# Optimization experiments

Hardware: AMD Instinct MI355X
Metric: run time of the kernel (lower is better)

The kernel has to match this reference:

```python
import jax, jax.numpy as jnp
import numpy as np


def _safe_inv(d):
    # 1/d with inf -> 0, as in PyG HypergraphConv
    return jnp.where(d > 0, 1.0 / jnp.maximum(d, 1e-30), 0.0)


def _hconv(x, W, b, node_idx, hedge_idx, num_hyperedges):
    """PyG HypergraphConv (use_attention=False, hyperedge_weight=1):
    out = D^-1 H B^-1 H^T (x W) + b
    """
    N = x.shape[0]
    xw = x @ W  # [N, F]
    ones = jnp.ones(node_idx.shape[0], dtype=x.dtype)
    D = _safe_inv(jax.ops.segment_sum(ones, node_idx, num_segments=N))
    B = _safe_inv(jax.ops.segment_sum(ones, hedge_idx, num_segments=num_hyperedges))
    # node -> hyperedge: mean of incident node features (norm B at target edge)
    e_feat = jax.ops.segment_sum(B[hedge_idx, None] * xw[node_idx], hedge_idx,
                                 num_segments=num_hyperedges)  # [M, F]
    # hyperedge -> node: degree-normalized sum (norm D at target node)
    out = jax.ops.segment_sum(D[node_idx, None] * e_feat[hedge_idx], node_idx,
                              num_segments=N)  # [N, F]
    return out + b


def _prelu(x, a):
    return jnp.where(x >= 0, x, a * x)


def setup_inputs() -> dict:
    key = jax.random.key(0)
    k = jax.random.split(key, 8)
    N, F, NNZ, M = 50000, 128, 800000, 5000
    x = jax.random.normal(k[0], (N, F), dtype=jnp.float32)
    node_idx = jax.random.randint(k[1], (NNZ,), 0, N)
    hedge_idx = jax.random.randint(k[2], (NNZ,), 0, M)
    scale = 1.0 / np.sqrt(F)
    W1 = jax.random.normal(k[3], (F, F), dtype=jnp.float32) * scale
    b1 = jnp.zeros((F,), dtype=jnp.float32)
    W2 = jax.random.normal(k[4], (F, F), dtype=jnp.float32) * scale
    b2 = jnp.zeros((F,), dtype=jnp.float32)
    prelu_a = jnp.asarray(0.25, dtype=jnp.float32)  # nn.PReLU default init
    return {"x": x, "W1": W1, "b1": b1, "W2": W2, "b2": b2,
            "prelu_a": prelu_a, "node_idx": node_idx, "hedge_idx": hedge_idx,
            "num_hyperedges": M}


def reference(x, W1, b1, W2, b2, prelu_a, node_idx, hedge_idx, num_hyperedges):
    out1 = _prelu(_hconv(x, W1, b1, node_idx, hedge_idx, num_hyperedges), prelu_a)
    out1 = _hconv(out1, W2, b2, node_idx, hedge_idx, num_hyperedges) + x
    return _prelu(out1, prelu_a)
```

## Files before the change

kernel.cpp:

```cpp
#include <hip/hip_runtime.h>


typedef __attribute__((ext_vector_type(8))) short bf16x8;
typedef __attribute__((ext_vector_type(4))) float f32x4;

#define CHUNK 4096

__device__ __forceinline__ float bf2f(ushort u) {
  union { uint i; float f; } v; v.i = ((uint)u) << 16; return v.f;
}
__device__ __forceinline__ ushort f2bf(float f) {
  union { uint i; float f; } v; v.f = f;
  uint b = v.i + 0x7FFFu + ((v.i >> 16) & 1u);
  return (ushort)(b >> 16);
}


__global__ __launch_bounds__(256) void init_cursors(int* __restrict__ cursH, int sbh,
                                                    int capH, int* __restrict__ cursN,
                                                    int sbn, int capN) {
  int t = threadIdx.x;
  if (t < sbh) cursH[t] = t * capH;
  if (t < sbn) cursN[t] = t * capN;
}

__global__ __launch_bounds__(256) void binA(const int* __restrict__ ni,
                                            const int* __restrict__ hi, int nnz,
                                            int* __restrict__ cursH,
                                            int* __restrict__ cursN,
                                            uint* __restrict__ tmpH,
                                            uint* __restrict__ tmpN,
                                            int sbh, int sbn) {
  __shared__ int hH[128], hN[128];
  int t = threadIdx.x, b = blockIdx.x;
  for (int i = t; i < sbh; i += 256) hH[i] = 0;
  for (int i = t; i < sbn; i += 256) hN[i] = 0;
  __syncthreads();
  int base = b * CHUNK;
  int lim = min(nnz, base + CHUNK);
  for (int i = base + t; i < lim; i += 256) {
    atomicAdd(&hH[hi[i] >> 6], 1);
    atomicAdd(&hN[ni[i] >> 9], 1);
  }
  __syncthreads();
  for (int i = t; i < sbh; i += 256) {
    int c = hH[i];
    hH[i] = c ? atomicAdd(&cursH[i], c) : 0;
  }
  for (int i = t; i < sbn; i += 256) {
    int c = hN[i];
    hN[i] = c ? atomicAdd(&cursN[i], c) : 0;
  }
  __syncthreads();
  for (int i = base + t; i < lim; i += 256) {
    uint n = (uint)ni[i], h = (uint)hi[i];
    int pH = atomicAdd(&hH[h >> 6], 1);
    tmpH[pH] = (h << 17) | n;
    int pN = atomicAdd(&hN[n >> 9], 1);
    tmpN[pN] = (n << 13) | h;
  }
}

__global__ __launch_bounds__(1024) void phaseB(
    const uint* __restrict__ tmpH, const int* __restrict__ cursH, int sbh, int capH,
    const uint* __restrict__ tmpN, const int* __restrict__ cursN, int sbn, int capN,
    int M, int N,
    uint* __restrict__ csrMn, int* __restrict__ offM, int* __restrict__ cntM,
    float* __restrict__ Bm,
    ushort* __restrict__ csrNh, int* __restrict__ offN, int* __restrict__ cntN,
    float* __restrict__ Dn) {
  __shared__ int hist[512], cur[512], wtot[8], wexcl8[8];
  int t = threadIdx.x, b = blockIdx.x, l = t & 63, w = t >> 6;
  if (b < sbh) {
    int base = b * capH;
    int end = cursH[b];
    if (t < 64) hist[t] = 0;
    __syncthreads();
    for (int i = base + t; i < end; i += 1024)
      atomicAdd(&hist[(tmpH[i] >> 17) & 63], 1);
    __syncthreads();
    if (t < 64) {
      int v = hist[t], x = v;
#pragma unroll
      for (int s = 1; s < 64; s <<= 1) {
        int u = __shfl_up(x, s, 64);
        if (t >= s) x += u;
      }
      int excl = x - v;
      int h = b * 64 + t;
      if (h < M) {
        offM[h] = base + excl;
        cntM[h] = v;
        Bm[h] = v > 0 ? 1.0f / (float)v : 0.0f;
      }
      cur[t] = base + excl;
    }
    __syncthreads();
    for (int i = base + t; i < end; i += 1024) {
      uint rec = tmpH[i];
      int pos = atomicAdd(&cur[(rec >> 17) & 63], 1);
      csrMn[pos] = rec & 0x1FFFFu;
    }
  } else {
    b -= sbh;
    int base = b * capN;
    int end = cursN[b];
    if (t < 512) hist[t] = 0;
    __syncthreads();
    for (int i = base + t; i < end; i += 1024)
      atomicAdd(&hist[(tmpN[i] >> 13) & 511], 1);
    __syncthreads();
    int v = 0, x = 0;
    if (t < 512) {
      v = hist[t]; x = v;
#pragma unroll
      for (int s = 1; s < 64; s <<= 1) {
        int u = __shfl_up(x, s, 64);
        if (l >= s) x += u;
      }
      if (l == 63) wtot[w] = x;
    }
    __syncthreads();
    if (t == 0) {
      int run = 0;
      for (int i = 0; i < 8; i++) { wexcl8[i] = run; run += wtot[i]; }
    }
    __syncthreads();
    if (t < 512) {
      int excl = wexcl8[w] + x - v;
      int n = b * 512 + t;
      if (n < N) {
        offN[n] = base + excl;
        cntN[n] = v;
        Dn[n] = v > 0 ? 1.0f / (float)v : 0.0f;
      }
      cur[t] = base + excl;
    }
    __syncthreads();
    for (int i = base + t; i < end; i += 1024) {
      uint rec = tmpN[i];
      int pos = atomicAdd(&cur[(rec >> 13) & 511], 1);
      csrNh[pos] = (ushort)(rec & 0x1FFFu);
    }
  }
}


__global__ __launch_bounds__(256) void convert_k(const float* __restrict__ x,
                                                 ushort* __restrict__ xb, int total) {
  int idx = (blockIdx.x * 256 + threadIdx.x) * 8;
  if (idx >= total) return;
  float4 f0 = *(const float4*)&x[idx];
  float4 f1 = *(const float4*)&x[idx + 4];
  bf16x8 o;
  o[0] = (short)f2bf(f0.x); o[1] = (short)f2bf(f0.y);
  o[2] = (short)f2bf(f0.z); o[3] = (short)f2bf(f0.w);
  o[4] = (short)f2bf(f1.x); o[5] = (short)f2bf(f1.y);
  o[6] = (short)f2bf(f1.z); o[7] = (short)f2bf(f1.w);
  *(bf16x8*)&xb[idx] = o;
}

__global__ __launch_bounds__(256) void edge_gather(const ushort* __restrict__ XIN,
                                                   const uint* __restrict__ src,
                                                   const int* __restrict__ off,
                                                   const int* __restrict__ cnt,
                                                   const float* __restrict__ Bm,
                                                   ushort* __restrict__ AGG, int M) {
  __shared__ float red[4][128];
  int t = threadIdx.x, w = t >> 6, l = t & 63;
  int g = t >> 4, s = t & 15;
  for (int m = blockIdx.x; m < M; m += gridDim.x) {
    int sb = off[m], e = sb + cnt[m];
    float acc[8];
#pragma unroll
    for (int j = 0; j < 8; j++) acc[j] = 0.f;
    int p = sb + g;
    for (; p + 16 < e; p += 32) {
      uint n0 = src[p], n1 = src[p + 16];
      bf16x8 v0 = *(const bf16x8*)&XIN[(size_t)n0 * 128 + s * 8];
      bf16x8 v1 = *(const bf16x8*)&XIN[(size_t)n1 * 128 + s * 8];
#pragma unroll
      for (int j = 0; j < 8; j++)
        acc[j] += bf2f((ushort)v0[j]) + bf2f((ushort)v1[j]);
    }
    if (p < e) {
      uint n0 = src[p];
      bf16x8 v0 = *(const bf16x8*)&XIN[(size_t)n0 * 128 + s * 8];
#pragma unroll
      for (int j = 0; j < 8; j++) acc[j] += bf2f((ushort)v0[j]);
    }
#pragma unroll
    for (int j = 0; j < 8; j++) {
      acc[j] += __shfl_xor(acc[j], 16, 64);
      acc[j] += __shfl_xor(acc[j], 32, 64);
    }
    if (l < 16) {
      *(float4*)&red[w][s * 8] = make_float4(acc[0], acc[1], acc[2], acc[3]);
      *(float4*)&red[w][s * 8 + 4] = make_float4(acc[4], acc[5], acc[6], acc[7]);
    }
    __syncthreads();
    if (t < 128) {
      float sum = red[0][t] + red[1][t] + red[2][t] + red[3][t];
      AGG[(size_t)m * 128 + t] = f2bf(Bm[m] * sum);
    }
    __syncthreads();
  }
}

__global__ __launch_bounds__(256) void gemm_mfma(const ushort* __restrict__ A,
                                                 const float* __restrict__ W,
                                                 ushort* __restrict__ Y, int N) {
  __shared__ ushort Wl[128 * 128];
  int t = threadIdx.x;
  for (int i = t * 4; i < 128 * 128; i += 1024) {
    float4 w4 = *(const float4*)&W[i];
    ushort4 u;
    u.x = f2bf(w4.x); u.y = f2bf(w4.y); u.z = f2bf(w4.z); u.w = f2bf(w4.w);
    *(ushort4*)&Wl[i] = u;
  }
  __syncthreads();
  int l = t & 63, wv = t >> 6;
  int wr = wv >> 1, wc = wv & 1;
  int lr = l & 15, lk = l >> 4;
  bf16x8 bf[4][4];
#pragma unroll
  for (int c = 0; c < 4; c++) {
    int col = wc * 64 + c * 16 + lr;
#pragma unroll
    for (int s = 0; s < 4; s++) {
      int k0 = s * 32 + lk * 8;
      bf16x8 v;
#pragma unroll
      for (int j = 0; j < 8; j++) v[j] = (short)Wl[(k0 + j) * 128 + col];
      bf[c][s] = v;
    }
  }
  int tiles = (N + 63) >> 6;
  for (int tile = blockIdx.x; tile < tiles; tile += gridDim.x) {
    f32x4 acc[2][4];
#pragma unroll
    for (int r = 0; r < 2; r++)
#pragma unroll
      for (int c = 0; c < 4; c++) acc[r][c] = (f32x4){0.f, 0.f, 0.f, 0.f};
    int rbase = tile * 64 + wr * 32;
#pragma unroll
    for (int s = 0; s < 4; s++) {
      int k0 = s * 32 + lk * 8;
      bf16x8 a[2];
#pragma unroll
      for (int r = 0; r < 2; r++) {
        int grow = rbase + r * 16 + lr;
        bf16x8 v = (bf16x8){0, 0, 0, 0, 0, 0, 0, 0};
        if (grow < N) v = *(const bf16x8*)&A[(size_t)grow * 128 + k0];
        a[r] = v;
      }
#pragma unroll
      for (int r = 0; r < 2; r++)
#pragma unroll
        for (int c = 0; c < 4; c++)
          acc[r][c] = __builtin_amdgcn_mfma_f32_16x16x32_bf16(a[r], bf[c][s],
                                                              acc[r][c], 0, 0, 0);
    }
#pragma unroll
    for (int r = 0; r < 2; r++)
#pragma unroll
      for (int c = 0; c < 4; c++)
#pragma unroll
        for (int j = 0; j < 4; j++) {
          int row = rbase + r * 16 + lk * 4 + j;
          int col = wc * 64 + c * 16 + lr;
          if (row < N) Y[(size_t)row * 128 + col] = f2bf(acc[r][c][j]);
        }
  }
}

template <bool RES>
__global__ __launch_bounds__(256) void node_gather(
    const ushort* __restrict__ EF, const ushort* __restrict__ srcH,
    const int* __restrict__ off, const int* __restrict__ cnt,
    const float* __restrict__ Dn, const float* __restrict__ bias,
    const float* __restrict__ addX, const float* __restrict__ pa,
    void* __restrict__ OUT, int N) {
  int t = threadIdx.x, w = t >> 6, l = t & 63;
  int n = blockIdx.x * 4 + w;
  if (n >= N) return;
  int g = l >> 4, s = l & 15;
  float acc[8];
#pragma unroll
  for (int j = 0; j < 8; j++) acc[j] = 0.f;
  int sb = off[n], e = sb + cnt[n];
  int p = sb + g;
  for (; p + 4 < e; p += 8) {
    int h0 = srcH[p], h1 = srcH[p + 4];
    bf16x8 v0 = *(const bf16x8*)&EF[(size_t)h0 * 128 + s * 8];
    bf16x8 v1 = *(const bf16x8*)&EF[(size_t)h1 * 128 + s * 8];
#pragma unroll
    for (int j = 0; j < 8; j++)
      acc[j] += bf2f((ushort)v0[j]) + bf2f((ushort)v1[j]);
  }
  if (p < e) {
    int h0 = srcH[p];
    bf16x8 v0 = *(const bf16x8*)&EF[(size_t)h0 * 128 + s * 8];
#pragma unroll
    for (int j = 0; j < 8; j++) acc[j] += bf2f((ushort)v0[j]);
  }
#pragma unroll
  for (int j = 0; j < 8; j++) {
    acc[j] += __shfl_xor(acc[j], 16, 64);
    acc[j] += __shfl_xor(acc[j], 32, 64);
  }
  if (g != 0) return;
  float d = Dn[n];
  float a = *pa;
  float r[8];
#pragma unroll
  for (int j = 0; j < 8; j++) r[j] = fmaf(acc[j], d, bias[s * 8 + j]);
  if constexpr (RES) {
    const float* xp = addX + (size_t)n * 128 + s * 8;
    float4 x0 = *(const float4*)xp;
    float4 x1 = *(const float4*)(xp + 4);
    r[0] += x0.x; r[1] += x0.y; r[2] += x0.z; r[3] += x0.w;
    r[4] += x1.x; r[5] += x1.y; r[6] += x1.z; r[7] += x1.w;
  }
#pragma unroll
  for (int j = 0; j < 8; j++) r[j] = r[j] >= 0.f ? r[j] : a * r[j];
  if constexpr (RES) {
    float* op = (float*)OUT + (size_t)n * 128 + s * 8;
    *(float4*)op = make_float4(r[0], r[1], r[2], r[3]);
    *(float4*)(op + 4) = make_float4(r[4], r[5], r[6], r[7]);
  } else {
    ushort* op = (ushort*)OUT + (size_t)n * 128 + s * 8;
    bf16x8 o;
#pragma unroll
    for (int j = 0; j < 8; j++) o[j] = (short)f2bf(r[j]);
    *(bf16x8*)op = o;
  }
}

extern "C" void kernel_launch(void* const* d_in, const int* in_sizes, int n_in,
                              void* d_out, int out_size, void* d_ws, size_t ws_size,
                              hipStream_t stream) {
  const float* x  = (const float*)d_in[0];
  const float* W1 = (const float*)d_in[1];
  const float* b1 = (const float*)d_in[2];
  const float* W2 = (const float*)d_in[3];
  const float* b2 = (const float*)d_in[4];
  const float* pa = (const float*)d_in[5];
  const int* ni   = (const int*)d_in[6];
  const int* hi   = (const int*)d_in[7];

  const int F = 128;
  const int N = in_sizes[0] / F;
  const int NNZ = in_sizes[6];
  const int M = 5000;

  const int NBA = (NNZ + CHUNK - 1) / CHUNK;
  const int SBH = (M + 63) / 64;
  const int SBN = (N + 511) / 512;
  int capH = (NNZ + SBH - 1) / SBH; capH += capH / 8 + 256; capH = (capH + 63) & ~63;
  int capN = (NNZ + SBN - 1) / SBN; capN += capN / 8 + 256; capN = (capN + 63) & ~63;

  char* p = (char*)d_ws;
  auto alloc = [&](size_t bytes) -> char* {
    char* r = p; p += (bytes + 255) & ~size_t(255); return r;
  };
  ushort* xb    = (ushort*)alloc(sizeof(ushort) * (size_t)N * F);
  ushort* h1    = (ushort*)alloc(sizeof(ushort) * (size_t)N * F);
  ushort* agg   = (ushort*)alloc(sizeof(ushort) * (size_t)M * F);
  ushort* ef    = (ushort*)alloc(sizeof(ushort) * (size_t)M * F);
  uint*   tmpH  = (uint*)alloc(sizeof(uint) * (size_t)SBH * capH);
  uint*   tmpN  = (uint*)alloc(sizeof(uint) * (size_t)SBN * capN);
  uint*   csrMn = (uint*)alloc(sizeof(uint) * (size_t)SBH * capH);
  ushort* csrNh = (ushort*)alloc(sizeof(ushort) * (size_t)SBN * capN);
  int*    offM  = (int*)alloc(sizeof(int) * M);
  int*    cntM  = (int*)alloc(sizeof(int) * M);
  int*    offN  = (int*)alloc(sizeof(int) * N);
  int*    cntN  = (int*)alloc(sizeof(int) * N);
  float*  Bm    = (float*)alloc(sizeof(float) * M);
  float*  Dn    = (float*)alloc(sizeof(float) * N);
  int*    cursH = (int*)alloc(sizeof(int) * SBH);
  int*    cursN = (int*)alloc(sizeof(int) * SBN);

  init_cursors<<<1, 256, 0, stream>>>(cursH, SBH, capH, cursN, SBN, capN);
  binA<<<NBA, 256, 0, stream>>>(ni, hi, NNZ, cursH, cursN, tmpH, tmpN, SBH, SBN);
  phaseB<<<SBH + SBN, 1024, 0, stream>>>(tmpH, cursH, SBH, capH,
                                         tmpN, cursN, SBN, capN, M, N,
                                         csrMn, offM, cntM, Bm,
                                         csrNh, offN, cntN, Dn);
  convert_k<<<(N * F / 8 + 255) / 256, 256, 0, stream>>>(x, xb, N * F);

  int etiles = (M + 63) / 64;
  edge_gather<<<M, 256, 0, stream>>>(xb, csrMn, offM, cntM, Bm, agg, M);
  gemm_mfma<<<etiles, 256, 0, stream>>>(agg, W1, ef, M);
  node_gather<false><<<(N + 3) / 4, 256, 0, stream>>>(ef, csrNh, offN, cntN, Dn,
                                                      b1, nullptr, pa, h1, N);
  edge_gather<<<M, 256, 0, stream>>>(h1, csrMn, offM, cntM, Bm, agg, M);
  gemm_mfma<<<etiles, 256, 0, stream>>>(agg, W2, ef, M);
  node_gather<true><<<(N + 3) / 4, 256, 0, stream>>>(ef, csrNh, offN, cntN, Dn,
                                                     b2, x, pa, (float*)d_out, N);
}
```

Baseline: 164.4 us.

## Fuse bf16 conversion into binning, unroll gathers, use bf16 residual

```diff
diff --git a/kernel.cpp b/kernel.cpp
--- a/kernel.cpp
+++ b/kernel.cpp
@@ -16,23 +16,28 @@
 }
 
 
-__global__ __launch_bounds__(256) void init_cursors(int* __restrict__ cursH, int sbh,
-                                                    int capH, int* __restrict__ cursN,
-                                                    int sbn, int capN) {
-  int t = threadIdx.x;
-  if (t < sbh) cursH[t] = t * capH;
-  if (t < sbn) cursN[t] = t * capN;
-}
-
-__global__ __launch_bounds__(256) void binA(const int* __restrict__ ni,
-                                            const int* __restrict__ hi, int nnz,
-                                            int* __restrict__ cursH,
-                                            int* __restrict__ cursN,
-                                            uint* __restrict__ tmpH,
-                                            uint* __restrict__ tmpN,
-                                            int sbh, int sbn) {
+__global__ __launch_bounds__(256) void binA_conv(
+    const int* __restrict__ ni, const int* __restrict__ hi, int nnz,
+    int* __restrict__ cursH, int* __restrict__ cursN,
+    uint* __restrict__ tmpH, uint* __restrict__ tmpN,
+    int sbh, int sbn, int capH, int capN, int nba,
+    const float* __restrict__ x, ushort* __restrict__ xb, int total) {
   __shared__ int hH[128], hN[128];
   int t = threadIdx.x, b = blockIdx.x;
+  if (b >= nba) {
+    int idx = ((b - nba) * 256 + t) * 8;
+    if (idx < total) {
+      float4 f0 = *(const float4*)&x[idx];
+      float4 f1 = *(const float4*)&x[idx + 4];
+      bf16x8 o;
+      o[0] = (short)f2bf(f0.x); o[1] = (short)f2bf(f0.y);
+      o[2] = (short)f2bf(f0.z); o[3] = (short)f2bf(f0.w);
+      o[4] = (short)f2bf(f1.x); o[5] = (short)f2bf(f1.y);
+      o[6] = (short)f2bf(f1.z); o[7] = (short)f2bf(f1.w);
+      *(bf16x8*)&xb[idx] = o;
+    }
+    return;
+  }
   for (int i = t; i < sbh; i += 256) hH[i] = 0;
   for (int i = t; i < sbn; i += 256) hN[i] = 0;
   __syncthreads();
@@ -45,11 +50,11 @@
   __syncthreads();
   for (int i = t; i < sbh; i += 256) {
     int c = hH[i];
-    hH[i] = c ? atomicAdd(&cursH[i], c) : 0;
+    hH[i] = c ? i * capH + atomicAdd(&cursH[i], c) : 0;
   }
   for (int i = t; i < sbn; i += 256) {
     int c = hN[i];
-    hN[i] = c ? atomicAdd(&cursN[i], c) : 0;
+    hN[i] = c ? i * capN + atomicAdd(&cursN[i], c) : 0;
   }
   __syncthreads();
   for (int i = base + t; i < lim; i += 256) {
@@ -73,7 +78,7 @@
   int t = threadIdx.x, b = blockIdx.x, l = t & 63, w = t >> 6;
   if (b < sbh) {
     int base = b * capH;
-    int end = cursH[b];
+    int end = base + cursH[b];
     if (t < 64) hist[t] = 0;
     __syncthreads();
     for (int i = base + t; i < end; i += 1024)
@@ -104,7 +109,7 @@
   } else {
     b -= sbh;
     int base = b * capN;
-    int end = cursN[b];
+    int end = base + cursN[b];
     if (t < 512) hist[t] = 0;
     __syncthreads();
     for (int i = base + t; i < end; i += 1024)
@@ -146,20 +151,6 @@
 }
 
 
-__global__ __launch_bounds__(256) void convert_k(const float* __restrict__ x,
-                                                 ushort* __restrict__ xb, int total) {
-  int idx = (blockIdx.x * 256 + threadIdx.x) * 8;
-  if (idx >= total) return;
-  float4 f0 = *(const float4*)&x[idx];
-  float4 f1 = *(const float4*)&x[idx + 4];
-  bf16x8 o;
-  o[0] = (short)f2bf(f0.x); o[1] = (short)f2bf(f0.y);
-  o[2] = (short)f2bf(f0.z); o[3] = (short)f2bf(f0.w);
-  o[4] = (short)f2bf(f1.x); o[5] = (short)f2bf(f1.y);
-  o[6] = (short)f2bf(f1.z); o[7] = (short)f2bf(f1.w);
-  *(bf16x8*)&xb[idx] = o;
-}
-
 __global__ __launch_bounds__(256) void edge_gather(const ushort* __restrict__ XIN,
                                                    const uint* __restrict__ src,
                                                    const int* __restrict__ off,
@@ -169,41 +160,50 @@
   __shared__ float red[4][128];
   int t = threadIdx.x, w = t >> 6, l = t & 63;
   int g = t >> 4, s = t & 15;
-  for (int m = blockIdx.x; m < M; m += gridDim.x) {
-    int sb = off[m], e = sb + cnt[m];
-    float acc[8];
-#pragma unroll
-    for (int j = 0; j < 8; j++) acc[j] = 0.f;
-    int p = sb + g;
-    for (; p + 16 < e; p += 32) {
-      uint n0 = src[p], n1 = src[p + 16];
-      bf16x8 v0 = *(const bf16x8*)&XIN[(size_t)n0 * 128 + s * 8];
-      bf16x8 v1 = *(const bf16x8*)&XIN[(size_t)n1 * 128 + s * 8];
-#pragma unroll
-      for (int j = 0; j < 8; j++)
-        acc[j] += bf2f((ushort)v0[j]) + bf2f((ushort)v1[j]);
-    }
-    if (p < e) {
-      uint n0 = src[p];
-      bf16x8 v0 = *(const bf16x8*)&XIN[(size_t)n0 * 128 + s * 8];
-#pragma unroll
-      for (int j = 0; j < 8; j++) acc[j] += bf2f((ushort)v0[j]);
-    }
-#pragma unroll
-    for (int j = 0; j < 8; j++) {
-      acc[j] += __shfl_xor(acc[j], 16, 64);
-      acc[j] += __shfl_xor(acc[j], 32, 64);
-    }
-    if (l < 16) {
-      *(float4*)&red[w][s * 8] = make_float4(acc[0], acc[1], acc[2], acc[3]);
-      *(float4*)&red[w][s * 8 + 4] = make_float4(acc[4], acc[5], acc[6], acc[7]);
-    }
-    __syncthreads();
-    if (t < 128) {
-      float sum = red[0][t] + red[1][t] + red[2][t] + red[3][t];
-      AGG[(size_t)m * 128 + t] = f2bf(Bm[m] * sum);
-    }
-    __syncthreads();
+  int m = blockIdx.x;
+  int sb = off[m], e = sb + cnt[m];
+  float acc[8];
+#pragma unroll
+  for (int j = 0; j < 8; j++) acc[j] = 0.f;
+  int p = sb + g;
+  for (; p + 48 < e; p += 64) {
+    uint n0 = src[p], n1 = src[p + 16], n2 = src[p + 32], n3 = src[p + 48];
+    bf16x8 v0 = *(const bf16x8*)&XIN[(size_t)n0 * 128 + s * 8];
+    bf16x8 v1 = *(const bf16x8*)&XIN[(size_t)n1 * 128 + s * 8];
+    bf16x8 v2 = *(const bf16x8*)&XIN[(size_t)n2 * 128 + s * 8];
+    bf16x8 v3 = *(const bf16x8*)&XIN[(size_t)n3 * 128 + s * 8];
+#pragma unroll
+    for (int j = 0; j < 8; j++)
+      acc[j] += (bf2f((ushort)v0[j]) + bf2f((ushort)v1[j])) +
+                (bf2f((ushort)v2[j]) + bf2f((ushort)v3[j]));
+  }
+  for (; p + 16 < e; p += 32) {
+    uint n0 = src[p], n1 = src[p + 16];
+    bf16x8 v0 = *(const bf16x8*)&XIN[(size_t)n0 * 128 + s * 8];
+    bf16x8 v1 = *(const bf16x8*)&XIN[(size_t)n1 * 128 + s * 8];
+#pragma unroll
+    for (int j = 0; j < 8; j++)
+      acc[j] += bf2f((ushort)v0[j]) + bf2f((ushort)v1[j]);
+  }
+  if (p < e) {
+    uint n0 = src[p];
+    bf16x8 v0 = *(const bf16x8*)&XIN[(size_t)n0 * 128 + s * 8];
+#pragma unroll
+    for (int j = 0; j < 8; j++) acc[j] += bf2f((ushort)v0[j]);
+  }
+#pragma unroll
+  for (int j = 0; j < 8; j++) {
+    acc[j] += __shfl_xor(acc[j], 16, 64);
+    acc[j] += __shfl_xor(acc[j], 32, 64);
+  }
+  if (l < 16) {
+    *(float4*)&red[w][s * 8] = make_float4(acc[0], acc[1], acc[2], acc[3]);
+    *(float4*)&red[w][s * 8 + 4] = make_float4(acc[4], acc[5], acc[6], acc[7]);
+  }
+  __syncthreads();
+  if (t < 128) {
+    float sum = red[0][t] + red[1][t] + red[2][t] + red[3][t];
+    AGG[(size_t)m * 128 + t] = f2bf(Bm[m] * sum);
   }
 }
 
@@ -279,7 +279,7 @@
     const ushort* __restrict__ EF, const ushort* __restrict__ srcH,
     const int* __restrict__ off, const int* __restrict__ cnt,
     const float* __restrict__ Dn, const float* __restrict__ bias,
-    const float* __restrict__ addX, const float* __restrict__ pa,
+    const ushort* __restrict__ addXb, const float* __restrict__ pa,
     void* __restrict__ OUT, int N) {
   int t = threadIdx.x, w = t >> 6, l = t & 63;
   int n = blockIdx.x * 4 + w;
@@ -290,6 +290,17 @@
   for (int j = 0; j < 8; j++) acc[j] = 0.f;
   int sb = off[n], e = sb + cnt[n];
   int p = sb + g;
+  for (; p + 12 < e; p += 16) {
+    int h0 = srcH[p], h1 = srcH[p + 4], h2 = srcH[p + 8], h3 = srcH[p + 12];
+    bf16x8 v0 = *(const bf16x8*)&EF[(size_t)h0 * 128 + s * 8];
+    bf16x8 v1 = *(const bf16x8*)&EF[(size_t)h1 * 128 + s * 8];
+    bf16x8 v2 = *(const bf16x8*)&EF[(size_t)h2 * 128 + s * 8];
+    bf16x8 v3 = *(const bf16x8*)&EF[(size_t)h3 * 128 + s * 8];
+#pragma unroll
+    for (int j = 0; j < 8; j++)
+      acc[j] += (bf2f((ushort)v0[j]) + bf2f((ushort)v1[j])) +
+                (bf2f((ushort)v2[j]) + bf2f((ushort)v3[j]));
+  }
   for (; p + 4 < e; p += 8) {
     int h0 = srcH[p], h1 = srcH[p + 4];
     bf16x8 v0 = *(const bf16x8*)&EF[(size_t)h0 * 128 + s * 8];
@@ -316,11 +327,9 @@
 #pragma unroll
   for (int j = 0; j < 8; j++) r[j] = fmaf(acc[j], d, bias[s * 8 + j]);
   if constexpr (RES) {
-    const float* xp = addX + (size_t)n * 128 + s * 8;
-    float4 x0 = *(const float4*)xp;
-    float4 x1 = *(const float4*)(xp + 4);
-    r[0] += x0.x; r[1] += x0.y; r[2] += x0.z; r[3] += x0.w;
-    r[4] += x1.x; r[5] += x1.y; r[6] += x1.z; r[7] += x1.w;
+    bf16x8 xv = *(const bf16x8*)&addXb[(size_t)n * 128 + s * 8];
+#pragma unroll
+    for (int j = 0; j < 8; j++) r[j] += bf2f((ushort)xv[j]);
   }
 #pragma unroll
   for (int j = 0; j < 8; j++) r[j] = r[j] >= 0.f ? r[j] : a * r[j];
@@ -378,16 +387,20 @@
   int*    cntN  = (int*)alloc(sizeof(int) * N);
   float*  Bm    = (float*)alloc(sizeof(float) * M);
   float*  Dn    = (float*)alloc(sizeof(float) * N);
-  int*    cursH = (int*)alloc(sizeof(int) * SBH);
-  int*    cursN = (int*)alloc(sizeof(int) * SBN);
-
-  init_cursors<<<1, 256, 0, stream>>>(cursH, SBH, capH, cursN, SBN, capN);
-  binA<<<NBA, 256, 0, stream>>>(ni, hi, NNZ, cursH, cursN, tmpH, tmpN, SBH, SBN);
+  int*    curs  = (int*)alloc(sizeof(int) * (SBH + SBN));
+  int*    cursH = curs;
+  int*    cursN = curs + SBH;
+
+  hipMemsetAsync(curs, 0, sizeof(int) * (SBH + SBN), stream);
+  int total = N * F;
+  int CONVB = (total / 8 + 255) / 256;
+  binA_conv<<<NBA + CONVB, 256, 0, stream>>>(ni, hi, NNZ, cursH, cursN,
+                                             tmpH, tmpN, SBH, SBN, capH, capN,
+                                             NBA, x, xb, total);
   phaseB<<<SBH + SBN, 1024, 0, stream>>>(tmpH, cursH, SBH, capH,
                                          tmpN, cursN, SBN, capN, M, N,
                                          csrMn, offM, cntM, Bm,
                                          csrNh, offN, cntN, Dn);
-  convert_k<<<(N * F / 8 + 255) / 256, 256, 0, stream>>>(x, xb, N * F);
 
   int etiles = (M + 63) / 64;
   edge_gather<<<M, 256, 0, stream>>>(xb, csrMn, offM, cntM, Bm, agg, M);
@@ -397,5 +410,5 @@
   edge_gather<<<M, 256, 0, stream>>>(h1, csrMn, offM, cntM, Bm, agg, M);
   gemm_mfma<<<etiles, 256, 0, stream>>>(agg, W2, ef, M);
   node_gather<true><<<(N + 3) / 4, 256, 0, stream>>>(ef, csrNh, offN, cntN, Dn,
-                                                     b2, x, pa, (float*)d_out, N);
-}
+                                                     b2, xb, pa, (float*)d_out, N);
+}
```

After: 162.8 us. No clear change (-1.0%).
